# Kernel tuning notes

Measured on AMD Instinct MI355X. Metric: run time of the kernel, lower is better.

Reference implementation:

```python
import jax, jax.numpy as jnp
import numpy as np

N = 300_000      # active voxels
L = 128          # occupied bounding grid side
M = 32           # unet width m
CIN = 3          # input_feature_number
NCLASS = 20
K = 27           # 3x3x3 submanifold kernel
BLOCK_REPS = 2
BN_EPS = 1e-4


def _build_neighbors(rng):
    """Rulebook: for each active voxel, index of each of its 27 neighbors (N = missing)."""
    coords = rng.integers(0, L, size=(int(N * 1.5), 3), dtype=np.int64)
    keys = coords[:, 0] * L * L + coords[:, 1] * L + coords[:, 2]
    keys = np.unique(keys)[:N]
    assert keys.shape[0] == N
    x = keys // (L * L); y = (keys // L) % L; z = keys % L
    c = np.stack([x, y, z], 1)                      # [N,3] sorted-by-key coords
    nbr = np.full((N, K), N, dtype=np.int32)
    k = 0
    for dx in (-1, 0, 1):
        for dy in (-1, 0, 1):
            for dz in (-1, 0, 1):
                nc = c + np.array([dx, dy, dz])
                valid = ((nc >= 0) & (nc < L)).all(1)
                nk = nc[:, 0] * L * L + nc[:, 1] * L + nc[:, 2]
                pos = np.searchsorted(keys, nk).clip(0, N - 1)
                found = valid & (keys[pos] == nk)
                nbr[:, k] = np.where(found, pos, N).astype(np.int32)
                k += 1
    return nbr


def setup_inputs() -> dict:
    rng = np.random.default_rng(0)
    nbr_idx = jnp.asarray(_build_neighbors(rng))
    key = jax.random.key(0)
    ks = jax.random.split(key, 16)
    s = 0.1
    inp = {
        "features": jax.random.normal(ks[0], (N, CIN), jnp.float32),
        "nbr_idx": nbr_idx,
        # initial SubmanifoldConvolution(3, m, 3, bias=False)
        "w0": jax.random.normal(ks[1], (K, CIN, M), jnp.float32) * s,
        # residual tower params: [rep, conv_in_block(2), ...]
        "bw": jax.random.normal(ks[2], (BLOCK_REPS, 2, K, M, M), jnp.float32) * s,
        "bg": jnp.ones((BLOCK_REPS, 2, M), jnp.float32),
        "bb": jnp.zeros((BLOCK_REPS, 2, M), jnp.float32),
        # final BatchNormReLU(m)
        "gf": jnp.ones((M,), jnp.float32),
        "bf": jnp.zeros((M,), jnp.float32),
        # dense heads
        "w_cls": jax.random.normal(ks[3], (M, NCLASS), jnp.float32) * s,
        "b_cls": jnp.zeros((NCLASS,), jnp.float32),
        "w_fe": jax.random.normal(ks[4], (M, M), jnp.float32) * s,
        "b_fe": jnp.zeros((M,), jnp.float32),
        "w_le": jax.random.normal(ks[5], (M, M), jnp.float32) * s,
        "b_le": jnp.zeros((M,), jnp.float32),
        "w_fr": jax.random.normal(ks[6], (M, M), jnp.float32) * s,
        "b_fr": jnp.zeros((M,), jnp.float32),
        "w_lr": jax.random.normal(ks[7], (M, 1), jnp.float32) * s,
        "b_lr": jnp.zeros((1,), jnp.float32),
    }
    return inp


def _subconv(feat, nbr, W):
    # feat [N,Cin], nbr [N,27] with sentinel N -> zero row, W [27,Cin,Cout]
    fpad = jnp.concatenate([feat, jnp.zeros((1, feat.shape[1]), feat.dtype)], 0)
    gathered = fpad[nbr]                       # [N,27,Cin] irregular gather
    return jnp.einsum('nkc,kcd->nd', gathered, W)


def _bn(x, g, b):
    mu = x.mean(0)
    var = ((x - mu) ** 2).mean(0)
    return (x - mu) * jax.lax.rsqrt(var + BN_EPS) * g + b


def reference(features, nbr_idx, w0, bw, bg, bb, gf, bf,
              w_cls, b_cls, w_fe, b_fe, w_le, b_le, w_fr, b_fr, w_lr, b_lr):
    feat = _subconv(features, nbr_idx, w0)     # [N,M]
    for r in range(BLOCK_REPS):                # pre-activation residual blocks
        h = _subconv(jax.nn.relu(_bn(feat, bg[r, 0], bb[r, 0])), nbr_idx, bw[r, 0])
        h = _subconv(jax.nn.relu(_bn(h, bg[r, 1], bb[r, 1])), nbr_idx, bw[r, 1])
        feat = feat + h
    feat = jax.nn.relu(_bn(feat, gf, bf))      # BatchNormReLU(m) + OutputLayer
    y = feat @ w_cls + b_cls                                   # [N,20]
    embedding = (feat @ w_fe + b_fe) @ w_le + b_le             # [N,32]
    offset = jax.nn.sigmoid((feat @ w_fr + b_fr) @ w_lr + b_lr)  # [N,1]
    return (y, embedding, offset)
```

## Files before the change

### kernel.cpp

```cpp
#include <hip/hip_runtime.h>

#define NVOX 300000
#define K27 27
#define VPB 128
#define TILES 2

typedef __attribute__((ext_vector_type(8))) __bf16 bf16x8;
typedef __attribute__((ext_vector_type(8))) unsigned short ushort8;
typedef __attribute__((ext_vector_type(4))) float f32x4;

__device__ inline unsigned short f2bf(float x){
  unsigned int u = __float_as_uint(x);
  unsigned int r = (u + 0x7FFFu + ((u >> 16) & 1u)) >> 16;
  return (unsigned short)r;
}

__global__ void pack_w_kernel(const float* __restrict__ bw, const float* __restrict__ w0,
                              unsigned short* __restrict__ pw, unsigned short* __restrict__ pw0){
  int t = blockIdx.x*256 + threadIdx.x;
  if (t < 4*K27*2*64){
    int l  = t & 63;
    int h  = (t >> 6) & 1;
    int k  = (t >> 7) % K27;
    int cv = t / (128*K27);
    int g = l >> 4, r16 = l & 15;
    ushort8 o;
    #pragma unroll
    for (int i = 0; i < 8; ++i){
      int c  = g*8 + i;
      int oc = h*16 + r16;
      o[i] = f2bf(bw[(((cv*K27 + k)*32) + c)*32 + oc]);
    }
    *reinterpret_cast<ushort8*>(pw + t*8) = o;
    return;
  }
  int u = t - 4*K27*2*64;
  if (u >= 4*2*64) return;
  int l  = u & 63;
  int h  = (u >> 6) & 1;
  int kb = u >> 7;
  int g = l >> 4, r16 = l & 15;
  int col = h*16 + r16;
  ushort8 o;
  #pragma unroll
  for (int i = 0; i < 8; ++i){
    int k   = kb*32 + g*8 + i;
    int tap = k >> 2, ch = k & 3;
    float v = (tap < K27 && ch < 3) ? w0[(tap*3 + ch)*32 + col] : 0.f;
    o[i] = f2bf(v);
  }
  *reinterpret_cast<ushort8*>(pw0 + u*8) = o;
}

__global__ void pack_hw_kernel(const float* __restrict__ w_cls, const float* __restrict__ b_cls,
                               const float* __restrict__ w_fe,  const float* __restrict__ b_fe,
                               const float* __restrict__ w_le,
                               const float* __restrict__ w_fr,  const float* __restrict__ b_fr,
                               unsigned short* __restrict__ pwh, float* __restrict__ bcat){
  int t = blockIdx.x*512 + threadIdx.x;
  if (t < 96){
    float v = 0.f;
    if (t < 32)      v = b_fe[t];
    else if (t < 64) v = b_fr[t-32];
    else if (t < 84) v = b_cls[t-64];
    bcat[t] = v;
  }
  if (t >= 8*64) return;
  int l = t & 63, f = t >> 6;
  int g = l >> 4, r16 = l & 15;
  ushort8 o;
  #pragma unroll
  for (int i = 0; i < 8; ++i){
    int k = g*8 + i;
    float v;
    if (f < 6){
      int col = f*16 + r16;
      if (col < 32)      v = w_fe[k*32 + col];
      else if (col < 64) v = w_fr[k*32 + (col-32)];
      else { int c = col - 64; v = (c < 20) ? w_cls[k*20 + c] : 0.f; }
    } else {
      int col = (f-6)*16 + r16;
      v = w_le[k*32 + col];
    }
    o[i] = f2bf(v);
  }
  *reinterpret_cast<ushort8*>(pwh + t*8) = o;
}

__global__ void prepad_kernel(const float* __restrict__ feats, float4* __restrict__ fpad){
  int row = blockIdx.x*256 + threadIdx.x;
  if (row > NVOX) return;
  float4 v = {0.f, 0.f, 0.f, 0.f};
  if (row < NVOX){
    v.x = feats[row*3+0]; v.y = feats[row*3+1]; v.z = feats[row*3+2];
  }
  fpad[row] = v;
}

__global__ void __launch_bounds__(256) conv0_mfma_kernel(
    const float4* __restrict__ fpad, const int* __restrict__ nbr,
    const unsigned short* __restrict__ pw0, float* __restrict__ trunk,
    float* __restrict__ stats){
  __shared__ int   snbr[256*K27];
  __shared__ float sstat[64];
  int tid  = threadIdx.x;
  int base = blockIdx.x*256;
  for (int i = tid; i < 256*K27; i += 256){
    int v = base + i / K27;
    snbr[i] = (v < NVOX) ? nbr[base*K27 + i] : NVOX;
  }
  if (tid < 64) sstat[tid] = 0.f;
  __syncthreads();

  int l = tid & 63, w = tid >> 6;
  int g = l >> 4, r16 = l & 15;
  const int vb = w*64;

  bf16x8 B[4][2];
  #pragma unroll
  for (int kb = 0; kb < 4; ++kb)
    #pragma unroll
    for (int h = 0; h < 2; ++h)
      B[kb][h] = *reinterpret_cast<const bf16x8*>(pw0 + (kb*2 + h)*512 + l*8);

  f32x4 acc[4][2];
  #pragma unroll
  for (int t = 0; t < 4; ++t)
    #pragma unroll
    for (int h = 0; h < 2; ++h)
      acc[t][h] = (f32x4){0.f,0.f,0.f,0.f};

  #pragma unroll
  for (int t = 0; t < 4; ++t){
    int row = (vb + t*16 + r16)*K27;
    #pragma unroll
    for (int kb = 0; kb < 4; ++kb){
      int tap0 = kb*8 + g*2;
      int tap1 = tap0 + 1;
      int i0 = (tap0 < K27) ? tap0 : 0;
      int i1 = (tap1 < K27) ? tap1 : 0;
      int j0 = snbr[row + i0]; if (tap0 >= K27) j0 = NVOX;
      int j1 = snbr[row + i1]; if (tap1 >= K27) j1 = NVOX;
      float4 v0 = fpad[j0];
      float4 v1 = fpad[j1];
      ushort8 au;
      au[0] = f2bf(v0.x); au[1] = f2bf(v0.y); au[2] = f2bf(v0.z); au[3] = 0;
      au[4] = f2bf(v1.x); au[5] = f2bf(v1.y); au[6] = f2bf(v1.z); au[7] = 0;
      bf16x8 a = __builtin_bit_cast(bf16x8, au);
      acc[t][0] = __builtin_amdgcn_mfma_f32_16x16x32_bf16(a, B[kb][0], acc[t][0], 0, 0, 0);
      acc[t][1] = __builtin_amdgcn_mfma_f32_16x16x32_bf16(a, B[kb][1], acc[t][1], 0, 0, 0);
    }
  }

  float s0[2] = {0.f, 0.f}, s1[2] = {0.f, 0.f};
  #pragma unroll
  for (int t = 0; t < 4; ++t){
    #pragma unroll
    for (int r = 0; r < 4; ++r){
      int row = base + vb + t*16 + g*4 + r;
      if (row < NVOX){
        #pragma unroll
        for (int h = 0; h < 2; ++h){
          float v = acc[t][h][r];
          trunk[(size_t)row*32 + h*16 + r16] = v;
          s0[h] += v; s1[h] += v*v;
        }
      }
    }
  }
  #pragma unroll
  for (int h = 0; h < 2; ++h){
    s0[h] += __shfl_xor(s0[h], 16);
    s0[h] += __shfl_xor(s0[h], 32);
    s1[h] += __shfl_xor(s1[h], 16);
    s1[h] += __shfl_xor(s1[h], 32);
  }
  if (l < 16){
    atomicAdd(&sstat[r16],      s0[0]);
    atomicAdd(&sstat[32 + r16], s1[0]);
    atomicAdd(&sstat[16 + r16], s0[1]);
    atomicAdd(&sstat[48 + r16], s1[1]);
  }
  __syncthreads();
  if (tid < 64) atomicAdd(&stats[(blockIdx.x & 63)*64 + tid], sstat[tid]);
}

__global__ void __launch_bounds__(256) act_kernel(
    const float* __restrict__ trunk, const float* __restrict__ stats,
    const float* __restrict__ g, const float* __restrict__ b,
    unsigned short* __restrict__ act){
  __shared__ float sbnp[64];
  int tid = threadIdx.x;
  if (tid < 32){
    float s = 0.f, q = 0.f;
    #pragma unroll
    for (int i = 0; i < 64; ++i){ s += stats[i*64 + tid]; q += stats[i*64 + 32 + tid]; }
    float inv = 1.0f / (float)NVOX;
    float mu  = s * inv;
    float var = q * inv - mu*mu;
    float sc  = g[tid] * rsqrtf(var + 1e-4f);
    sbnp[tid]      = sc;
    sbnp[32 + tid] = b[tid] - mu*sc;
  }
  __syncthreads();

  int t = blockIdx.x*256 + tid;
  if (t >= (NVOX+1)*4) return;
  int row = t >> 2, part = t & 3;
  ushort8 o;
  if (row < NVOX){
    const float* p = trunk + (size_t)row*32 + part*8;
    #pragma unroll
    for (int i = 0; i < 8; ++i){
      float v = p[i]*sbnp[part*8 + i] + sbnp[32 + part*8 + i];
      v = fmaxf(v, 0.f);
      o[i] = f2bf(v);
    }
  } else {
    #pragma unroll
    for (int i = 0; i < 8; ++i) o[i] = 0;
  }
  *reinterpret_cast<ushort8*>(act + (size_t)row*32 + part*8) = o;
}

template<bool RES>
__global__ void __launch_bounds__(256) conv_mfma_kernel(
    const unsigned short* __restrict__ act, const int* __restrict__ nbr,
    const unsigned short* __restrict__ pw, float* __restrict__ trunk,
    float* __restrict__ stats){
  __shared__ int   snbr[VPB*K27];
  __shared__ float sstat[64];
  int tid  = threadIdx.x;
  int base = blockIdx.x*VPB;
  for (int i = tid; i < VPB*K27; i += 256){
    int v = base + i / K27;
    snbr[i] = (v < NVOX) ? nbr[(size_t)base*K27 + i] : NVOX;
  }
  if (tid < 64) sstat[tid] = 0.f;
  __syncthreads();

  int l = tid & 63, w = tid >> 6;
  int g = l >> 4, r16 = l & 15;
  const int vb = w*(TILES*16);

  int rb[TILES];
  #pragma unroll
  for (int t = 0; t < TILES; ++t) rb[t] = (vb + t*16 + r16)*K27;

  f32x4 acc[TILES][2];
  #pragma unroll
  for (int t = 0; t < TILES; ++t)
    #pragma unroll
    for (int h = 0; h < 2; ++h)
      acc[t][h] = (f32x4){0.f,0.f,0.f,0.f};

  #pragma unroll
  for (int k = 0; k < K27; ++k){
    bf16x8 b0 = *reinterpret_cast<const bf16x8*>(pw + (k*2    )*512 + l*8);
    bf16x8 b1 = *reinterpret_cast<const bf16x8*>(pw + (k*2 + 1)*512 + l*8);
    bf16x8 a[TILES];
    #pragma unroll
    for (int t = 0; t < TILES; ++t){
      int j = snbr[rb[t] + k];
      a[t] = *reinterpret_cast<const bf16x8*>(act + (size_t)j*32 + g*8);
    }
    #pragma unroll
    for (int t = 0; t < TILES; ++t){
      acc[t][0] = __builtin_amdgcn_mfma_f32_16x16x32_bf16(a[t], b0, acc[t][0], 0, 0, 0);
      acc[t][1] = __builtin_amdgcn_mfma_f32_16x16x32_bf16(a[t], b1, acc[t][1], 0, 0, 0);
    }
  }

  float s0[2] = {0.f, 0.f}, s1[2] = {0.f, 0.f};
  #pragma unroll
  for (int t = 0; t < TILES; ++t){
    #pragma unroll
    for (int r = 0; r < 4; ++r){
      int row = base + vb + t*16 + g*4 + r;
      if (row < NVOX){
        #pragma unroll
        for (int h = 0; h < 2; ++h){
          float v = acc[t][h][r];
          float* p = trunk + (size_t)row*32 + h*16 + r16;
          if (RES) v += *p;
          *p = v;
          s0[h] += v; s1[h] += v*v;
        }
      }
    }
  }
  #pragma unroll
  for (int h = 0; h < 2; ++h){
    s0[h] += __shfl_xor(s0[h], 16);
    s0[h] += __shfl_xor(s0[h], 32);
    s1[h] += __shfl_xor(s1[h], 16);
    s1[h] += __shfl_xor(s1[h], 32);
  }
  if (l < 16){
    atomicAdd(&sstat[r16],      s0[0]);
    atomicAdd(&sstat[32 + r16], s1[0]);
    atomicAdd(&sstat[16 + r16], s0[1]);
    atomicAdd(&sstat[48 + r16], s1[1]);
  }
  __syncthreads();
  if (tid < 64) atomicAdd(&stats[(blockIdx.x & 63)*64 + tid], sstat[tid]);
}

__global__ void __launch_bounds__(256) heads_mfma_kernel(
    const float* __restrict__ trunk, const float* __restrict__ stats,
    const float* __restrict__ gf, const float* __restrict__ bf,
    const unsigned short* __restrict__ pwh, const float* __restrict__ bcat,
    const float* __restrict__ b_le, const float* __restrict__ w_lr, const float* __restrict__ b_lr,
    float* __restrict__ out){
  __shared__ float lds[4][16][33];
  __shared__ float sbnp[64];
  int tid = threadIdx.x;
  if (tid < 32){
    float s = 0.f, q = 0.f;
    #pragma unroll
    for (int i = 0; i < 64; ++i){ s += stats[i*64 + tid]; q += stats[i*64 + 32 + tid]; }
    float inv = 1.0f / (float)NVOX;
    float mu  = s * inv;
    float var = q * inv - mu*mu;
    float sc  = gf[tid] * rsqrtf(var + 1e-4f);
    sbnp[tid]      = sc;
    sbnp[32 + tid] = bf[tid] - mu*sc;
  }
  __syncthreads();

  int l = tid & 63, w = tid >> 6;
  int g = l >> 4, r16 = l & 15;
  int base = blockIdx.x*256 + w*64;

  bf16x8 B1[6], B2[2];
  #pragma unroll
  for (int f = 0; f < 6; ++f)
    B1[f] = *reinterpret_cast<const bf16x8*>(pwh + f*512 + l*8);
  #pragma unroll
  for (int h = 0; h < 2; ++h)
    B2[h] = *reinterpret_cast<const bf16x8*>(pwh + (6+h)*512 + l*8);

  float sc[8], bi[8];
  #pragma unroll
  for (int i = 0; i < 8; ++i){ sc[i] = sbnp[g*8 + i]; bi[i] = sbnp[32 + g*8 + i]; }
  float wlr0 = w_lr[r16], wlr1 = w_lr[16 + r16];
  float blr  = b_lr[0];
  float bc0  = bcat[r16],      bc1  = bcat[16 + r16];
  float bc2  = bcat[32 + r16], bc3  = bcat[48 + r16];
  float bc4  = bcat[64 + r16], bc5  = bcat[80 + r16];
  float ble0 = b_le[r16],      ble1 = b_le[16 + r16];

  float* out_e = out + (size_t)NVOX*20;
  float* out_o = out + (size_t)NVOX*52;

  for (int t = 0; t < 4; ++t){
    int arow = base + t*16 + r16;
    float4 fa = {0.f,0.f,0.f,0.f}, fb2 = {0.f,0.f,0.f,0.f};
    if (arow < NVOX){
      fa  = *reinterpret_cast<const float4*>(trunk + (size_t)arow*32 + g*8);
      fb2 = *reinterpret_cast<const float4*>(trunk + (size_t)arow*32 + g*8 + 4);
    }
    ushort8 au;
    au[0] = f2bf(fmaxf(fa.x*sc[0] + bi[0], 0.f));
    au[1] = f2bf(fmaxf(fa.y*sc[1] + bi[1], 0.f));
    au[2] = f2bf(fmaxf(fa.z*sc[2] + bi[2], 0.f));
    au[3] = f2bf(fmaxf(fa.w*sc[3] + bi[3], 0.f));
    au[4] = f2bf(fmaxf(fb2.x*sc[4] + bi[4], 0.f));
    au[5] = f2bf(fmaxf(fb2.y*sc[5] + bi[5], 0.f));
    au[6] = f2bf(fmaxf(fb2.z*sc[6] + bi[6], 0.f));
    au[7] = f2bf(fmaxf(fb2.w*sc[7] + bi[7], 0.f));
    bf16x8 a = __builtin_bit_cast(bf16x8, au);

    f32x4 acc[6];
    #pragma unroll
    for (int j = 0; j < 6; ++j){
      acc[j] = (f32x4){0.f,0.f,0.f,0.f};
      acc[j] = __builtin_amdgcn_mfma_f32_16x16x32_bf16(a, B1[j], acc[j], 0, 0, 0);
    }

    #pragma unroll
    for (int r = 0; r < 4; ++r){
      int orow = base + t*16 + g*4 + r;
      if (orow < NVOX){
        out[(size_t)orow*20 + r16] = acc[4][r] + bc4;
        if (r16 < 4)
          out[(size_t)orow*20 + 16 + r16] = acc[5][r] + bc5;
      }
    }

    float part[4];
    #pragma unroll
    for (int r = 0; r < 4; ++r)
      part[r] = (acc[2][r] + bc2)*wlr0 + (acc[3][r] + bc3)*wlr1;
    #pragma unroll
    for (int r = 0; r < 4; ++r){
      part[r] += __shfl_xor(part[r], 1);
      part[r] += __shfl_xor(part[r], 2);
      part[r] += __shfl_xor(part[r], 4);
      part[r] += __shfl_xor(part[r], 8);
    }
    if (r16 == 0){
      #pragma unroll
      for (int r = 0; r < 4; ++r){
        int orow = base + t*16 + g*4 + r;
        if (orow < NVOX)
          out_o[orow] = 1.f/(1.f + __expf(-(part[r] + blr)));
      }
    }

    #pragma unroll
    for (int r = 0; r < 4; ++r){
      lds[w][g*4 + r][r16]      = acc[0][r] + bc0;
      lds[w][g*4 + r][16 + r16] = acc[1][r] + bc1;
    }
    ushort8 a2u;
    #pragma unroll
    for (int i = 0; i < 8; ++i)
      a2u[i] = f2bf(lds[w][r16][g*8 + i]);
    bf16x8 a2 = __builtin_bit_cast(bf16x8, a2u);
    f32x4 e0 = (f32x4){0.f,0.f,0.f,0.f}, e1 = (f32x4){0.f,0.f,0.f,0.f};
    e0 = __builtin_amdgcn_mfma_f32_16x16x32_bf16(a2, B2[0], e0, 0, 0, 0);
    e1 = __builtin_amdgcn_mfma_f32_16x16x32_bf16(a2, B2[1], e1, 0, 0, 0);
    #pragma unroll
    for (int r = 0; r < 4; ++r){
      int orow = base + t*16 + g*4 + r;
      if (orow < NVOX){
        out_e[(size_t)orow*32 + r16]      = e0[r] + ble0;
        out_e[(size_t)orow*32 + 16 + r16] = e1[r] + ble1;
      }
    }
  }
}

extern "C" void kernel_launch(void* const* d_in, const int* in_sizes, int n_in,
                              void* d_out, int out_size, void* d_ws, size_t ws_size,
                              hipStream_t stream){
  const float* features = (const float*)d_in[0];
  const int*   nbr      = (const int*)  d_in[1];
  const float* w0       = (const float*)d_in[2];
  const float* bw       = (const float*)d_in[3];
  const float* bg       = (const float*)d_in[4];
  const float* bb       = (const float*)d_in[5];
  const float* gf       = (const float*)d_in[6];
  const float* bf       = (const float*)d_in[7];
  const float* w_cls    = (const float*)d_in[8];
  const float* b_cls    = (const float*)d_in[9];
  const float* w_fe     = (const float*)d_in[10];
  const float* b_fe     = (const float*)d_in[11];
  const float* w_le     = (const float*)d_in[12];
  const float* b_le     = (const float*)d_in[13];
  const float* w_fr     = (const float*)d_in[14];
  const float* b_fr     = (const float*)d_in[15];
  const float* w_lr     = (const float*)d_in[16];
  const float* b_lr     = (const float*)d_in[17];
  float* out = (float*)d_out;

  char* ws = (char*)d_ws;
  float*          trunkA = (float*)(ws);
  float*          trunkH = (float*)(ws + 38400000);
  float4*         fpad   = (float4*)(ws + 38400000);
  unsigned short* actB   = (unsigned short*)(ws + 76800000);
  unsigned short* pw     = (unsigned short*)(ws + 96000128);
  unsigned short* pw0    = (unsigned short*)(ws + 96221312);
  float*          stats  = (float*)(ws + 96229504);
  unsigned short* pwh    = (unsigned short*)(ws + 96311424);
  float*          bcat   = (float*)(ws + 96319616);

  hipMemsetAsync(stats, 0, 5*64*64*sizeof(float), stream);
  pack_w_kernel<<<(4*K27*2*64 + 4*2*64 + 255)/256, 256, 0, stream>>>(bw, w0, pw, pw0);
  pack_hw_kernel<<<1, 512, 0, stream>>>(w_cls, b_cls, w_fe, b_fe, w_le, w_fr, b_fr, pwh, bcat);
  prepad_kernel<<<(NVOX + 256)/256, 256, 0, stream>>>(features, fpad);

  const int NB  = (NVOX + 255)/256;
  const int NB2 = (NVOX + VPB - 1)/VPB;
  const int NA  = ((NVOX+1)*4 + 255)/256;

  conv0_mfma_kernel<<<NB, 256, 0, stream>>>(fpad, nbr, pw0, trunkA, stats + 0*4096);
  act_kernel<<<NA, 256, 0, stream>>>(trunkA, stats + 0*4096, bg +  0, bb +  0, actB);
  conv_mfma_kernel<false><<<NB2, 256, 0, stream>>>(actB, nbr, pw + 0*27648, trunkH, stats + 1*4096);
  act_kernel<<<NA, 256, 0, stream>>>(trunkH, stats + 1*4096, bg + 32, bb + 32, actB);
  conv_mfma_kernel<true ><<<NB2, 256, 0, stream>>>(actB, nbr, pw + 1*27648, trunkA, stats + 2*4096);
  act_kernel<<<NA, 256, 0, stream>>>(trunkA, stats + 2*4096, bg + 64, bb + 64, actB);
  conv_mfma_kernel<false><<<NB2, 256, 0, stream>>>(actB, nbr, pw + 2*27648, trunkH, stats + 3*4096);
  act_kernel<<<NA, 256, 0, stream>>>(trunkH, stats + 3*4096, bg + 96, bb + 96, actB);
  conv_mfma_kernel<true ><<<NB2, 256, 0, stream>>>(actB, nbr, pw + 3*27648, trunkA, stats + 4*4096);
  heads_mfma_kernel<<<NB, 256, 0, stream>>>(trunkA, stats + 4*4096, gf, bf, pwh, bcat,
                                            b_le, w_lr, b_lr, out);
}
```

Measured before the change: 450.8 us.

## Swizzle conv block order across XCDs and use nontemporal streaming accesses

Conv block indices are remapped so each group of eight interleaved block IDs covers one contiguous range of voxel chunks. The hardware spreads block IDs round-robin over eight XCDs, so this keeps spatially adjacent voxels, and their shared neighbor rows, in the same XCD's L2 during the irregular gathers. Grid sizes change to fixed block counts that fit the mapping, and conv0 gets an early exit for its padding blocks. Trunk, activation and rulebook reads and writes become nontemporal to limit cache pollution from streaming data. The risk is that these bypass hints also drop reuse between consecutive kernels.

```diff
diff --git a/kernel.cpp b/kernel.cpp
--- a/kernel.cpp
+++ b/kernel.cpp
@@ -4,6 +4,10 @@
 #define K27 27
 #define VPB 128
 #define TILES 2
+#define NBLK 2344
+#define CPX  (NBLK/8)
+#define NBLK0 1176
+#define CPX0 (NBLK0/8)
 
 typedef __attribute__((ext_vector_type(8))) __bf16 bf16x8;
 typedef __attribute__((ext_vector_type(8))) unsigned short ushort8;
@@ -87,10 +91,10 @@
   *reinterpret_cast<ushort8*>(pwh + t*8) = o;
 }
 
-__global__ void prepad_kernel(const float* __restrict__ feats, float4* __restrict__ fpad){
+__global__ void prepad_kernel(const float* __restrict__ feats, f32x4* __restrict__ fpad){
   int row = blockIdx.x*256 + threadIdx.x;
   if (row > NVOX) return;
-  float4 v = {0.f, 0.f, 0.f, 0.f};
+  f32x4 v = {0.f, 0.f, 0.f, 0.f};
   if (row < NVOX){
     v.x = feats[row*3+0]; v.y = feats[row*3+1]; v.z = feats[row*3+2];
   }
@@ -98,16 +102,20 @@
 }
 
 __global__ void __launch_bounds__(256) conv0_mfma_kernel(
-    const float4* __restrict__ fpad, const int* __restrict__ nbr,
+    const f32x4* __restrict__ fpad, const int* __restrict__ nbr,
     const unsigned short* __restrict__ pw0, float* __restrict__ trunk,
     float* __restrict__ stats){
+  int bid   = blockIdx.x;
+  int chunk = (bid & 7)*CPX0 + (bid >> 3);
+  int base  = chunk*256;
+  if (base >= NVOX) return;
+
   __shared__ int   snbr[256*K27];
   __shared__ float sstat[64];
-  int tid  = threadIdx.x;
-  int base = blockIdx.x*256;
+  int tid = threadIdx.x;
   for (int i = tid; i < 256*K27; i += 256){
     int v = base + i / K27;
-    snbr[i] = (v < NVOX) ? nbr[base*K27 + i] : NVOX;
+    snbr[i] = (v < NVOX) ? __builtin_nontemporal_load(&nbr[(size_t)base*K27 + i]) : NVOX;
   }
   if (tid < 64) sstat[tid] = 0.f;
   __syncthreads();
@@ -141,8 +149,8 @@
       int i1 = (tap1 < K27) ? tap1 : 0;
       int j0 = snbr[row + i0]; if (tap0 >= K27) j0 = NVOX;
       int j1 = snbr[row + i1]; if (tap1 >= K27) j1 = NVOX;
-      float4 v0 = fpad[j0];
-      float4 v1 = fpad[j1];
+      f32x4 v0 = fpad[j0];
+      f32x4 v1 = fpad[j1];
       ushort8 au;
       au[0] = f2bf(v0.x); au[1] = f2bf(v0.y); au[2] = f2bf(v0.z); au[3] = 0;
       au[4] = f2bf(v1.x); au[5] = f2bf(v1.y); au[6] = f2bf(v1.z); au[7] = 0;
@@ -162,7 +170,7 @@
         #pragma unroll
         for (int h = 0; h < 2; ++h){
           float v = acc[t][h][r];
-          trunk[(size_t)row*32 + h*16 + r16] = v;
+          __builtin_nontemporal_store(v, trunk + (size_t)row*32 + h*16 + r16);
           s0[h] += v; s1[h] += v*v;
         }
       }
@@ -209,10 +217,13 @@
   int row = t >> 2, part = t & 3;
   ushort8 o;
   if (row < NVOX){
-    const float* p = trunk + (size_t)row*32 + part*8;
+    const f32x4* p = reinterpret_cast<const f32x4*>(trunk + (size_t)row*32 + part*8);
+    f32x4 v0 = __builtin_nontemporal_load(p);
+    f32x4 v1 = __builtin_nontemporal_load(p + 1);
+    float vv[8] = {v0.x, v0.y, v0.z, v0.w, v1.x, v1.y, v1.z, v1.w};
     #pragma unroll
     for (int i = 0; i < 8; ++i){
-      float v = p[i]*sbnp[part*8 + i] + sbnp[32 + part*8 + i];
+      float v = vv[i]*sbnp[part*8 + i] + sbnp[32 + part*8 + i];
       v = fmaxf(v, 0.f);
       o[i] = f2bf(v);
     }
@@ -220,7 +231,7 @@
     #pragma unroll
     for (int i = 0; i < 8; ++i) o[i] = 0;
   }
-  *reinterpret_cast<ushort8*>(act + (size_t)row*32 + part*8) = o;
+  __builtin_nontemporal_store(o, reinterpret_cast<ushort8*>(act + (size_t)row*32 + part*8));
 }
 
 template<bool RES>
@@ -228,13 +239,16 @@
     const unsigned short* __restrict__ act, const int* __restrict__ nbr,
     const unsigned short* __restrict__ pw, float* __restrict__ trunk,
     float* __restrict__ stats){
+  int bid   = blockIdx.x;
+  int chunk = (bid & 7)*CPX + (bid >> 3);
+  const int base = chunk*VPB;
+
   __shared__ int   snbr[VPB*K27];
   __shared__ float sstat[64];
-  int tid  = threadIdx.x;
-  int base = blockIdx.x*VPB;
+  int tid = threadIdx.x;
   for (int i = tid; i < VPB*K27; i += 256){
     int v = base + i / K27;
-    snbr[i] = (v < NVOX) ? nbr[(size_t)base*K27 + i] : NVOX;
+    snbr[i] = (v < NVOX) ? __builtin_nontemporal_load(&nbr[(size_t)base*K27 + i]) : NVOX;
   }
   if (tid < 64) sstat[tid] = 0.f;
   __syncthreads();
@@ -282,8 +296,8 @@
         for (int h = 0; h < 2; ++h){
           float v = acc[t][h][r];
           float* p = trunk + (size_t)row*32 + h*16 + r16;
-          if (RES) v += *p;
-          *p = v;
+          if (RES) v += __builtin_nontemporal_load(p);
+          __builtin_nontemporal_store(v, p);
           s0[h] += v; s1[h] += v*v;
         }
       }
@@ -355,10 +369,11 @@
 
   for (int t = 0; t < 4; ++t){
     int arow = base + t*16 + r16;
-    float4 fa = {0.f,0.f,0.f,0.f}, fb2 = {0.f,0.f,0.f,0.f};
+    f32x4 fa = {0.f,0.f,0.f,0.f}, fb2 = {0.f,0.f,0.f,0.f};
     if (arow < NVOX){
-      fa  = *reinterpret_cast<const float4*>(trunk + (size_t)arow*32 + g*8);
-      fb2 = *reinterpret_cast<const float4*>(trunk + (size_t)arow*32 + g*8 + 4);
+      const f32x4* p = reinterpret_cast<const f32x4*>(trunk + (size_t)arow*32 + g*8);
+      fa  = __builtin_nontemporal_load(p);
+      fb2 = __builtin_nontemporal_load(p + 1);
     }
     ushort8 au;
     au[0] = f2bf(fmaxf(fa.x*sc[0] + bi[0], 0.f));
@@ -458,7 +473,7 @@
   char* ws = (char*)d_ws;
   float*          trunkA = (float*)(ws);
   float*          trunkH = (float*)(ws + 38400000);
-  float4*         fpad   = (float4*)(ws + 38400000);
+  f32x4*          fpad   = (f32x4*)(ws + 38400000);
   unsigned short* actB   = (unsigned short*)(ws + 76800000);
   unsigned short* pw     = (unsigned short*)(ws + 96000128);
   unsigned short* pw0    = (unsigned short*)(ws + 96221312);
@@ -472,18 +487,17 @@
   prepad_kernel<<<(NVOX + 256)/256, 256, 0, stream>>>(features, fpad);
 
   const int NB  = (NVOX + 255)/256;
-  const int NB2 = (NVOX + VPB - 1)/VPB;
   const int NA  = ((NVOX+1)*4 + 255)/256;
 
-  conv0_mfma_kernel<<<NB, 256, 0, stream>>>(fpad, nbr, pw0, trunkA, stats + 0*4096);
+  conv0_mfma_kernel<<<NBLK0, 256, 0, stream>>>(fpad, nbr, pw0, trunkA, stats + 0*4096);
   act_kernel<<<NA, 256, 0, stream>>>(trunkA, stats + 0*4096, bg +  0, bb +  0, actB);
-  conv_mfma_kernel<false><<<NB2, 256, 0, stream>>>(actB, nbr, pw + 0*27648, trunkH, stats + 1*4096);
+  conv_mfma_kernel<false><<<NBLK, 256, 0, stream>>>(actB, nbr, pw + 0*27648, trunkH, stats + 1*4096);
   act_kernel<<<NA, 256, 0, stream>>>(trunkH, stats + 1*4096, bg + 32, bb + 32, actB);
-  conv_mfma_kernel<true ><<<NB2, 256, 0, stream>>>(actB, nbr, pw + 1*27648, trunkA, stats + 2*4096);
+  conv_mfma_kernel<true ><<<NBLK, 256, 0, stream>>>(actB, nbr, pw + 1*27648, trunkA, stats + 2*4096);
   act_kernel<<<NA, 256, 0, stream>>>(trunkA, stats + 2*4096, bg + 64, bb + 64, actB);
-  conv_mfma_kernel<false><<<NB2, 256, 0, stream>>>(actB, nbr, pw + 2*27648, trunkH, stats + 3*4096);
+  conv_mfma_kernel<false><<<NBLK, 256, 0, stream>>>(actB, nbr, pw + 2*27648, trunkH, stats + 3*4096);
   act_kernel<<<NA, 256, 0, stream>>>(trunkH, stats + 3*4096, bg + 96, bb + 96, actB);
-  conv_mfma_kernel<true ><<<NB2, 256, 0, stream>>>(actB, nbr, pw + 3*27648, trunkA, stats + 4*4096);
+  conv_mfma_kernel<true ><<<NBLK, 256, 0, stream>>>(actB, nbr, pw + 3*27648, trunkA, stats + 4*4096);
   heads_mfma_kernel<<<NB, 256, 0, stream>>>(trunkA, stats + 4*4096, gf, bf, pwh, bcat,
                                             b_le, w_lr, b_lr, out);
 }
```

New measurement: 548.7 us. 1.22x slower.
